# Performance work log

Hardware: AMD Instinct MI355X
Metric: run time of the kernel (lower is better)

Reference implementation:

```python
import jax, jax.numpy as jnp
import numpy as np

SEQ, BATCH, IN, H = 2048, 1024, 10, 20


def setup_inputs() -> dict:
    key = jax.random.key(0)
    ks = jax.random.split(key, 11)
    s = 1.0 / np.sqrt(H)  # PyTorch LSTM init range
    u = lambda k, shape: jax.random.uniform(k, shape, jnp.float32, -s, s)
    return {
        "x": jax.random.normal(ks[0], (SEQ, BATCH, IN), jnp.float32),
        "h0": jax.random.normal(ks[1], (2, BATCH, H), jnp.float32),
        "c0": jax.random.normal(ks[2], (2, BATCH, H), jnp.float32),
        "w_ih_f": u(ks[3], (4 * H, IN)),
        "w_hh_f": u(ks[4], (4 * H, H)),
        "b_ih_f": u(ks[5], (4 * H,)),
        "b_hh_f": u(ks[6], (4 * H,)),
        "w_ih_b": u(ks[7], (4 * H, IN)),
        "w_hh_b": u(ks[8], (4 * H, H)),
        "b_ih_b": u(ks[9], (4 * H,)),
        "b_hh_b": u(ks[10], (4 * H,)),
    }


def _scan_dir(x_proj, h0, c0, w_hh):
    # x_proj: [seq, batch, 4H] precomputed input projection + biases
    def step(carry, g_in):
        h, c = carry
        g = g_in + h @ w_hh.T  # [batch, 4H]
        i, f, gg, o = jnp.split(g, 4, axis=-1)  # PyTorch gate order i,f,g,o
        c = jax.nn.sigmoid(f) * c + jax.nn.sigmoid(i) * jnp.tanh(gg)
        h = jax.nn.sigmoid(o) * jnp.tanh(c)
        return (h, c), h

    (hT, cT), hs = jax.lax.scan(step, (h0, c0), x_proj)
    return hs, hT, cT


def reference(x, h0, c0, w_ih_f, w_hh_f, b_ih_f, b_hh_f, w_ih_b, w_hh_b, b_ih_b, b_hh_b):
    # forward direction
    xf = jnp.einsum('sbi,gi->sbg', x, w_ih_f) + (b_ih_f + b_hh_f)
    hs_f, hT_f, cT_f = _scan_dir(xf, h0[0], c0[0], w_hh_f)
    # backward direction: scan over time-reversed sequence, then flip outputs
    xb = jnp.einsum('sbi,gi->sbg', x[::-1], w_ih_b) + (b_ih_b + b_hh_b)
    hs_b, hT_b, cT_b = _scan_dir(xb, h0[1], c0[1], w_hh_b)
    hs_b = hs_b[::-1]
    out = jnp.concatenate([hs_f, hs_b], axis=-1)  # [seq, batch, 2H]
    h_n = jnp.stack([hT_f, hT_b])  # [2, batch, H]
    c_n = jnp.stack([cT_f, cT_b])
    return out, h_n, c_n
```

## Files before the change

kernel.cpp:

```cpp
#include <hip/hip_runtime.h>

namespace {

constexpr int SEQ = 2048, BATCH = 1024, IN = 10, H = 20;
constexpr int WB   = 3;
constexpr int NBLK = (BATCH + WB - 1) / WB;
constexpr int XS   = 32;
constexpr float L2E = 1.4426950408889634f;

typedef _Float16 h2t __attribute__((ext_vector_type(2)));

__device__ __forceinline__ float rcpf(float x) { return __builtin_amdgcn_rcpf(x); }
__device__ __forceinline__ float xp2(float x) {
#if __has_builtin(__builtin_amdgcn_exp2f)
    return __builtin_amdgcn_exp2f(x);
#else
    return exp2f(x);
#endif
}
__device__ __forceinline__ int pk(float a, float b) {
    auto v = __builtin_amdgcn_cvt_pkrtz(a, b);
    int i; __builtin_memcpy(&i, &v, 4); return i;
}
__device__ __forceinline__ float dot2(int a, int b, float c) {
    h2t ha, hb; __builtin_memcpy(&ha, &a, 4); __builtin_memcpy(&hb, &b, 4);
#if __has_builtin(__builtin_amdgcn_fdot2)
    return __builtin_amdgcn_fdot2(ha, hb, c, false);
#else
    return c + (float)ha.x * (float)hb.x + (float)ha.y * (float)hb.y;
#endif
}

__launch_bounds__(64)
__global__ void lstm_bidir(const float* __restrict__ x,
                           const float* __restrict__ h0,
                           const float* __restrict__ c0,
                           const float* __restrict__ w_ih_f, const float* __restrict__ w_hh_f,
                           const float* __restrict__ b_ih_f, const float* __restrict__ b_hh_f,
                           const float* __restrict__ w_ih_b, const float* __restrict__ w_hh_b,
                           const float* __restrict__ b_ih_b, const float* __restrict__ b_hh_b,
                           float* __restrict__ out, float* __restrict__ h_n, float* __restrict__ c_n)
{
    const int dir  = blockIdx.y;
    const int b0   = blockIdx.x * WB;
    const int lane = threadIdx.x;
    int slot = lane / H; if (slot >= WB) slot = WB - 1;
    const int u    = lane % H;
    const bool active = (lane < WB * H) && (b0 + lane / H < BATCH);
    const int b    = min(b0 + slot, BATCH - 1);

    const float* w_ih = dir ? w_ih_b : w_ih_f;
    const float* w_hh = dir ? w_hh_b : w_hh_f;
    const float* bi   = dir ? b_ih_b : b_ih_f;
    const float* bh   = dir ? b_hh_b : b_hh_f;

    __shared__ __align__(16) float   xlds[2][XS][32];
    __shared__ __align__(16) _Float16 hlds[WB * 24];

    int wh[4][10], wi[4][5]; float bias[4];
    #pragma unroll
    for (int q = 0; q < 4; ++q) {
        const float sc = (q == 2) ? (-2.0f * L2E) : (-L2E);
        const int g = q * H + u;
        #pragma unroll
        for (int k = 0; k < 10; ++k)
            wh[q][k] = pk(w_hh[g * H + 2 * k] * sc, w_hh[g * H + 2 * k + 1] * sc);
        #pragma unroll
        for (int k = 0; k < 5; ++k)
            wi[q][k] = pk(w_ih[g * IN + 2 * k] * sc, w_ih[g * IN + 2 * k + 1] * sc);
        bias[q] = (bi[g] + bh[g]) * sc;
    }

    float c  = c0[(dir * BATCH + b) * H + u];
    float hv = h0[(dir * BATCH + b) * H + u];

    float4 pend[4];
    const int t_ss = lane >> 3;
    const int t_c4 = (lane & 7) * 4;
    auto issue_chunk = [&](int s0) {
        #pragma unroll
        for (int t = 0; t < 4; ++t) {
            const int ss   = t * 8 + t_ss;
            const int srow = s0 + ss;
            const int xrow = dir ? (SEQ - 1 - srow) : srow;
            const int gcol = min(b0 * IN + t_c4, BATCH * IN - 4);
            pend[t] = *(const float4*)(x + (size_t)xrow * (BATCH * IN) + gcol);
        }
    };
    auto write_chunk = [&](int buf) {
        #pragma unroll
        for (int t = 0; t < 4; ++t)
            *(float4*)&xlds[buf][t * 8 + t_ss][t_c4] = pend[t];
    };
    const int lastfix = (b0 * IN + 32 > BATCH * IN) ? 1 : 0;

    issue_chunk(0);  write_chunk(0);
    issue_chunk(XS);

    float*          optr  = out + (size_t)(dir ? SEQ - 1 : 0) * (BATCH * 2 * H) + b * (2 * H) + dir * H + u;
    const ptrdiff_t ostep = dir ? -(ptrdiff_t)(BATCH * 2 * H) : (ptrdiff_t)(BATCH * 2 * H);

    const int hown = slot * 24 + u;
    const _Float16* hsl = &hlds[0] + slot * 24;

    for (int s0 = 0; s0 < SEQ; s0 += XS) {
        const int buf = (s0 / XS) & 1;
        for (int ss = 0; ss < XS; ++ss) {
            hlds[hown] = (_Float16)hv;
            const int4 p03 = *(const int4*)(hsl);
            const int4 p47 = *(const int4*)(hsl + 8);
            const int2 p89 = *(const int2*)(hsl + 16);

            const float2* xp = (const float2*)&xlds[buf][ss][slot * 10];
            const float2 a0 = xp[0], a1 = xp[1], a2 = xp[2], a3 = xp[3], a4 = xp[4 + lastfix];
            int xq[5];
            xq[0] = pk(a0.x, a0.y); xq[1] = pk(a1.x, a1.y); xq[2] = pk(a2.x, a2.y);
            xq[3] = pk(a3.x, a3.y); xq[4] = pk(a4.x, a4.y);

            int hp[10];
            hp[0]=p03.x; hp[1]=p03.y; hp[2]=p03.z; hp[3]=p03.w;
            hp[4]=p47.x; hp[5]=p47.y; hp[6]=p47.z; hp[7]=p47.w;
            hp[8]=p89.x; hp[9]=p89.y;

            float acc[4];
            #pragma unroll
            for (int q = 0; q < 4; ++q) {
                float a = bias[q];
                #pragma unroll
                for (int k = 0; k < 10; ++k) a = dot2(hp[k], wh[q][k], a);
                #pragma unroll
                for (int k = 0; k < 5; ++k)  a = dot2(xq[k], wi[q][k], a);
                acc[q] = a;
            }

            const float gi = rcpf(1.0f + xp2(acc[0]));
            const float gf = rcpf(1.0f + xp2(acc[1]));
            const float gt = fmaf(2.0f, rcpf(1.0f + xp2(acc[2])), -1.0f);
            const float go = rcpf(1.0f + xp2(acc[3]));
            c = fmaf(gf, c, gi * gt);
            const float th = fmaf(2.0f, rcpf(1.0f + xp2(c * (-2.0f * L2E))), -1.0f);
            hv = go * th;

            if (active) __builtin_nontemporal_store(hv, optr);
            optr += ostep;
        }
        if (s0 + XS < SEQ) {
            write_chunk(buf ^ 1);
            if (s0 + 2 * XS < SEQ) issue_chunk(s0 + 2 * XS);
        }
    }

    if (active) {
        h_n[(dir * BATCH + b) * H + u] = hv;
        c_n[(dir * BATCH + b) * H + u] = c;
    }
}

}

extern "C" void kernel_launch(void* const* d_in, const int* in_sizes, int n_in,
                              void* d_out, int out_size, void* d_ws, size_t ws_size,
                              hipStream_t stream)
{
    const float* x      = (const float*)d_in[0];
    const float* h0     = (const float*)d_in[1];
    const float* c0     = (const float*)d_in[2];
    const float* w_ih_f = (const float*)d_in[3];
    const float* w_hh_f = (const float*)d_in[4];
    const float* b_ih_f = (const float*)d_in[5];
    const float* b_hh_f = (const float*)d_in[6];
    const float* w_ih_b = (const float*)d_in[7];
    const float* w_hh_b = (const float*)d_in[8];
    const float* b_ih_b = (const float*)d_in[9];
    const float* b_hh_b = (const float*)d_in[10];

    float* out = (float*)d_out;
    float* h_n = out + (size_t)SEQ * BATCH * 2 * H;
    float* c_n = h_n + (size_t)2 * BATCH * H;

    dim3 grid(NBLK, 2), block(64);
    hipLaunchKernelGGL(lstm_bidir, grid, block, 0, stream,
                       x, h0, c0, w_ih_f, w_hh_f, b_ih_f, b_hh_f,
                       w_ih_b, w_hh_b, b_ih_b, b_hh_b, out, h_n, c_n);
}
```

Baseline: 606.5 us.

## Split gate computation across lane pairs with one batch row per wave

```diff
diff --git a/kernel.cpp b/kernel.cpp
--- a/kernel.cpp
+++ b/kernel.cpp
@@ -3,32 +3,27 @@
 namespace {
 
 constexpr int SEQ = 2048, BATCH = 1024, IN = 10, H = 20;
-constexpr int WB   = 3;
-constexpr int NBLK = (BATCH + WB - 1) / WB;
-constexpr int XS   = 32;
+constexpr int XS  = 32;
+constexpr int XROW = 12;
 constexpr float L2E = 1.4426950408889634f;
 
 typedef _Float16 h2t __attribute__((ext_vector_type(2)));
 
 __device__ __forceinline__ float rcpf(float x) { return __builtin_amdgcn_rcpf(x); }
-__device__ __forceinline__ float xp2(float x) {
-#if __has_builtin(__builtin_amdgcn_exp2f)
-    return __builtin_amdgcn_exp2f(x);
-#else
-    return exp2f(x);
-#endif
-}
+__device__ __forceinline__ float xp2(float x)  { return __builtin_amdgcn_exp2f(x); }
+
 __device__ __forceinline__ int pk(float a, float b) {
     auto v = __builtin_amdgcn_cvt_pkrtz(a, b);
     int i; __builtin_memcpy(&i, &v, 4); return i;
 }
 __device__ __forceinline__ float dot2(int a, int b, float c) {
     h2t ha, hb; __builtin_memcpy(&ha, &a, 4); __builtin_memcpy(&hb, &b, 4);
-#if __has_builtin(__builtin_amdgcn_fdot2)
     return __builtin_amdgcn_fdot2(ha, hb, c, false);
-#else
-    return c + (float)ha.x * (float)hb.x + (float)ha.y * (float)hb.y;
-#endif
+}
+__device__ __forceinline__ float dpp_x1(float v) {
+    int i; __builtin_memcpy(&i, &v, 4);
+    int r = __builtin_amdgcn_update_dpp(0, i, 0xB1, 0xF, 0xF, true);
+    float f; __builtin_memcpy(&f, &r, 4); return f;
 }
 
 __launch_bounds__(64)
@@ -42,117 +37,122 @@
                            float* __restrict__ out, float* __restrict__ h_n, float* __restrict__ c_n)
 {
     const int dir  = blockIdx.y;
-    const int b0   = blockIdx.x * WB;
+    const int b    = blockIdx.x;
     const int lane = threadIdx.x;
-    int slot = lane / H; if (slot >= WB) slot = WB - 1;
-    const int u    = lane % H;
-    const bool active = (lane < WB * H) && (b0 + lane / H < BATCH);
-    const int b    = min(b0 + slot, BATCH - 1);
+    const int u    = lane >> 1;
+    const int gp   = lane & 1;
+    const int ur   = (u < H) ? u : (H - 1);
+    const bool red = (gp == 0) && (u < H);
 
     const float* w_ih = dir ? w_ih_b : w_ih_f;
     const float* w_hh = dir ? w_hh_b : w_hh_f;
     const float* bi   = dir ? b_ih_b : b_ih_f;
     const float* bh   = dir ? b_hh_b : b_hh_f;
 
-    __shared__ __align__(16) float   xlds[2][XS][32];
-    __shared__ __align__(16) _Float16 hlds[WB * 24];
+    __shared__ __align__(16) float    xlds[2][XS * XROW];
+    __shared__ __align__(16) _Float16 hlds[32];
 
-    int wh[4][10], wi[4][5]; float bias[4];
+    const int g0 = gp * 2 * H + ur, g1 = g0 + H;
+    const float sc0 = gp ? (-2.0f * L2E) : (-L2E);
+    const float sc1 = -L2E;
+    const float na0 = gp ? 2.0f : 1.0f;
+    const float nd0 = gp ? -1.0f : 0.0f;
+
+    int wh[2][10], wi[2][5]; float bias[2];
     #pragma unroll
-    for (int q = 0; q < 4; ++q) {
-        const float sc = (q == 2) ? (-2.0f * L2E) : (-L2E);
-        const int g = q * H + u;
+    for (int k = 0; k < 10; ++k) {
+        wh[0][k] = pk(w_hh[g0 * H + 2 * k] * sc0, w_hh[g0 * H + 2 * k + 1] * sc0);
+        wh[1][k] = pk(w_hh[g1 * H + 2 * k] * sc1, w_hh[g1 * H + 2 * k + 1] * sc1);
+    }
+    #pragma unroll
+    for (int k = 0; k < 5; ++k) {
+        wi[0][k] = pk(w_ih[g0 * IN + 2 * k] * sc0, w_ih[g0 * IN + 2 * k + 1] * sc0);
+        wi[1][k] = pk(w_ih[g1 * IN + 2 * k] * sc1, w_ih[g1 * IN + 2 * k + 1] * sc1);
+    }
+    bias[0] = (bi[g0] + bh[g0]) * sc0;
+    bias[1] = (bi[g1] + bh[g1]) * sc1;
+
+    float c  = c0[(dir * BATCH + b) * H + ur];
+    float hv = h0[(dir * BATCH + b) * H + ur];
+    hlds[u] = (_Float16)hv;
+
+    const float*    xbase = x + (size_t)(dir ? SEQ - 1 : 0) * (BATCH * IN) + b * IN;
+    const ptrdiff_t xstep = dir ? -(ptrdiff_t)(BATCH * IN) : (ptrdiff_t)(BATCH * IN);
+
+    const float* xaddr[5];  int wadd[5];
+    #pragma unroll
+    for (int i = 0; i < 5; ++i) {
+        const int e = lane + 64 * i;
+        xaddr[i] = xbase + (ptrdiff_t)(e / 10) * xstep + (e % 10);
+        wadd[i]  = (e / 10) * XROW + (e % 10);
+    }
+    float pend[5];
+    auto issue_chunk = [&]() {
         #pragma unroll
-        for (int k = 0; k < 10; ++k)
-            wh[q][k] = pk(w_hh[g * H + 2 * k] * sc, w_hh[g * H + 2 * k + 1] * sc);
+        for (int i = 0; i < 5; ++i) pend[i] = *xaddr[i];
         #pragma unroll
-        for (int k = 0; k < 5; ++k)
-            wi[q][k] = pk(w_ih[g * IN + 2 * k] * sc, w_ih[g * IN + 2 * k + 1] * sc);
-        bias[q] = (bi[g] + bh[g]) * sc;
-    }
-
-    float c  = c0[(dir * BATCH + b) * H + u];
-    float hv = h0[(dir * BATCH + b) * H + u];
-
-    float4 pend[4];
-    const int t_ss = lane >> 3;
-    const int t_c4 = (lane & 7) * 4;
-    auto issue_chunk = [&](int s0) {
-        #pragma unroll
-        for (int t = 0; t < 4; ++t) {
-            const int ss   = t * 8 + t_ss;
-            const int srow = s0 + ss;
-            const int xrow = dir ? (SEQ - 1 - srow) : srow;
-            const int gcol = min(b0 * IN + t_c4, BATCH * IN - 4);
-            pend[t] = *(const float4*)(x + (size_t)xrow * (BATCH * IN) + gcol);
-        }
+        for (int i = 0; i < 5; ++i) xaddr[i] += XS * xstep;
     };
     auto write_chunk = [&](int buf) {
+        float* dst = &xlds[buf][0];
         #pragma unroll
-        for (int t = 0; t < 4; ++t)
-            *(float4*)&xlds[buf][t * 8 + t_ss][t_c4] = pend[t];
+        for (int i = 0; i < 5; ++i) dst[wadd[i]] = pend[i];
     };
-    const int lastfix = (b0 * IN + 32 > BATCH * IN) ? 1 : 0;
 
-    issue_chunk(0);  write_chunk(0);
-    issue_chunk(XS);
+    issue_chunk();  write_chunk(0);
+    issue_chunk();
 
-    float*          optr  = out + (size_t)(dir ? SEQ - 1 : 0) * (BATCH * 2 * H) + b * (2 * H) + dir * H + u;
+    float*          optr  = out + (size_t)(dir ? SEQ - 1 : 0) * (BATCH * 2 * H) + b * (2 * H) + dir * H + ur;
     const ptrdiff_t ostep = dir ? -(ptrdiff_t)(BATCH * 2 * H) : (ptrdiff_t)(BATCH * 2 * H);
 
-    const int hown = slot * 24 + u;
-    const _Float16* hsl = &hlds[0] + slot * 24;
+    for (int s0 = 0; s0 < SEQ; s0 += XS) {
+        const int buf = (s0 >> 5) & 1;
+        const float* xrowp = &xlds[buf][0];
+        for (int ss = 0; ss < XS; ++ss) {
+            const int4 hA = *(const int4*)(&hlds[0]);
+            const int4 hB = *(const int4*)(&hlds[8]);
+            const int2 hC = *(const int2*)(&hlds[16]);
+            const float4 xa = *(const float4*)(xrowp);
+            const float4 xb = *(const float4*)(xrowp + 4);
+            const float2 xc = *(const float2*)(xrowp + 8);
+            xrowp += XROW;
 
-    for (int s0 = 0; s0 < SEQ; s0 += XS) {
-        const int buf = (s0 / XS) & 1;
-        for (int ss = 0; ss < XS; ++ss) {
-            hlds[hown] = (_Float16)hv;
-            const int4 p03 = *(const int4*)(hsl);
-            const int4 p47 = *(const int4*)(hsl + 8);
-            const int2 p89 = *(const int2*)(hsl + 16);
+            int hp[10] = { hA.x, hA.y, hA.z, hA.w, hB.x, hB.y, hB.z, hB.w, hC.x, hC.y };
+            int xq[5]  = { pk(xa.x, xa.y), pk(xa.z, xa.w), pk(xb.x, xb.y), pk(xb.z, xb.w), pk(xc.x, xc.y) };
 
-            const float2* xp = (const float2*)&xlds[buf][ss][slot * 10];
-            const float2 a0 = xp[0], a1 = xp[1], a2 = xp[2], a3 = xp[3], a4 = xp[4 + lastfix];
-            int xq[5];
-            xq[0] = pk(a0.x, a0.y); xq[1] = pk(a1.x, a1.y); xq[2] = pk(a2.x, a2.y);
-            xq[3] = pk(a3.x, a3.y); xq[4] = pk(a4.x, a4.y);
+            float a0 = bias[0], a1 = bias[1];
+            #pragma unroll
+            for (int k = 0; k < 10; ++k) { a0 = dot2(hp[k], wh[0][k], a0); a1 = dot2(hp[k], wh[1][k], a1); }
+            #pragma unroll
+            for (int k = 0; k < 5;  ++k) { a0 = dot2(xq[k], wi[0][k], a0); a1 = dot2(xq[k], wi[1][k], a1); }
 
-            int hp[10];
-            hp[0]=p03.x; hp[1]=p03.y; hp[2]=p03.z; hp[3]=p03.w;
-            hp[4]=p47.x; hp[5]=p47.y; hp[6]=p47.z; hp[7]=p47.w;
-            hp[8]=p89.x; hp[9]=p89.y;
+            const float n0 = fmaf(na0, rcpf(1.0f + xp2(a0)), nd0);
+            const float n1 = rcpf(1.0f + xp2(a1));
 
-            float acc[4];
-            #pragma unroll
-            for (int q = 0; q < 4; ++q) {
-                float a = bias[q];
-                #pragma unroll
-                for (int k = 0; k < 10; ++k) a = dot2(hp[k], wh[q][k], a);
-                #pragma unroll
-                for (int k = 0; k < 5; ++k)  a = dot2(xq[k], wi[q][k], a);
-                acc[q] = a;
-            }
+            const float m0 = dpp_x1(n0);
+            const float m1 = dpp_x1(n1);
+            const float gi = gp ? m0 : n0;
+            const float gf = gp ? m1 : n1;
+            const float gt = gp ? n0 : m0;
+            const float go = gp ? n1 : m1;
 
-            const float gi = rcpf(1.0f + xp2(acc[0]));
-            const float gf = rcpf(1.0f + xp2(acc[1]));
-            const float gt = fmaf(2.0f, rcpf(1.0f + xp2(acc[2])), -1.0f);
-            const float go = rcpf(1.0f + xp2(acc[3]));
             c = fmaf(gf, c, gi * gt);
             const float th = fmaf(2.0f, rcpf(1.0f + xp2(c * (-2.0f * L2E))), -1.0f);
             hv = go * th;
 
-            if (active) __builtin_nontemporal_store(hv, optr);
+            hlds[u] = (_Float16)hv;
+            if (red) __builtin_nontemporal_store(hv, optr);
             optr += ostep;
         }
         if (s0 + XS < SEQ) {
             write_chunk(buf ^ 1);
-            if (s0 + 2 * XS < SEQ) issue_chunk(s0 + 2 * XS);
+            if (s0 + 2 * XS < SEQ) issue_chunk();
         }
     }
 
-    if (active) {
-        h_n[(dir * BATCH + b) * H + u] = hv;
-        c_n[(dir * BATCH + b) * H + u] = c;
+    if (red) {
+        h_n[(dir * BATCH + b) * H + ur] = hv;
+        c_n[(dir * BATCH + b) * H + ur] = c;
     }
 }
 
@@ -178,7 +178,7 @@
     float* h_n = out + (size_t)SEQ * BATCH * 2 * H;
     float* c_n = h_n + (size_t)2 * BATCH * H;
 
-    dim3 grid(NBLK, 2), block(64);
+    dim3 grid(BATCH, 2), block(64);
     hipLaunchKernelGGL(lstm_bidir, grid, block, 0, stream,
                        x, h0, c0, w_ih_f, w_hh_f, b_ih_f, b_hh_f,
                        w_ih_b, w_hh_b, b_ih_b, b_hh_b, out, h_n, c_n);
```

After: 653.2 us. 7.7% more time.
